# Kernel optimization log

Measured on AMD Instinct MI355X. Metric: run time of the kernel, lower is better.

The kernel has to match this reference:

```python
import jax, jax.numpy as jnp
import numpy as np

N = 100000      # nodes
E = 1600000     # edges
G = 2000        # molecules (graphs)
F = 40          # node features
FE = 16         # edge features
H = 64          # conv width
HM = 128        # mlp width
C = 2           # classes
NEG_SLOPE = 0.01
BN_EPS = 1e-5


def leaky(x):
    return jnp.where(x >= 0, x, NEG_SLOPE * x)


def batch_norm(x, g, b):
    # training-mode BatchNorm over the node axis (biased variance, eps=1e-5)
    m = jnp.mean(x, axis=0)
    v = jnp.var(x, axis=0)
    return (x - m) * jax.lax.rsqrt(v + BN_EPS) * g + b


def setup_inputs() -> dict:
    key = jax.random.key(0)
    ks = iter(jax.random.split(key, 100))

    def nrm(shape, s=1.0):
        return jax.random.normal(next(ks), shape, dtype=jnp.float32) * s

    inp = {}
    inp["x"] = nrm((N, F))
    inp["edge_index"] = jax.random.randint(next(ks), (2, E), 0, N, dtype=jnp.int32)
    inp["edge_attr"] = nrm((E, FE))
    inp["batch"] = jnp.repeat(jnp.arange(G, dtype=jnp.int32), N // G)

    dims = [(F, H), (H, H), (H, H)]
    for i, (ci, co) in enumerate(dims):
        inp[f"conv{i}_eps"] = jnp.zeros((1,), dtype=jnp.float32)
        inp[f"conv{i}_We"] = nrm((FE, ci), 1.0 / np.sqrt(FE))
        inp[f"conv{i}_be"] = nrm((ci,), 0.05)
        inp[f"conv{i}_W1"] = nrm((ci, co), 1.0 / np.sqrt(ci))
        inp[f"conv{i}_b1"] = nrm((co,), 0.05)
        inp[f"conv{i}_g1"] = 1.0 + nrm((co,), 0.05)
        inp[f"conv{i}_bt1"] = nrm((co,), 0.05)
        inp[f"conv{i}_W2"] = nrm((co, co), 1.0 / np.sqrt(co))
        inp[f"conv{i}_b2"] = nrm((co,), 0.05)
        inp[f"bn{i}_g"] = 1.0 + nrm((co,), 0.05)
        inp[f"bn{i}_b"] = nrm((co,), 0.05)

    inp["mlp0_W"] = nrm((2 * H, HM), 1.0 / np.sqrt(2 * H))
    inp["mlp0_b"] = nrm((HM,), 0.05)
    inp["mlp1_W"] = nrm((HM, HM), 1.0 / np.sqrt(HM))
    inp["mlp1_b"] = nrm((HM,), 0.05)
    inp["final_W"] = nrm((HM, C), 1.0 / np.sqrt(HM))
    inp["final_b"] = nrm((C,), 0.05)
    return inp


def _forward(x, edge_attr, edge_index, batch, convs, mlps, final_W, final_b):
    src, dst = edge_index[0], edge_index[1]
    for (eps, We, be, W1, b1, g1, bt1, W2, b2, bg, bb) in convs:
        # GINEConv: msg = relu(x_src + lin_edge(edge_attr)); scatter-add to dst
        e = edge_attr @ We + be                    # [E, in]
        msg = jax.nn.relu(x[src] + e)              # gather + fuse
        agg = jax.ops.segment_sum(msg, dst, num_segments=x.shape[0])
        h = (1.0 + eps) * x + agg
        # conv nn: Linear -> BatchNorm -> LeakyReLU -> Linear
        h = batch_norm(h @ W1 + b1, g1, bt1)
        h = leaky(h) @ W2 + b2
        # outer BatchNorm + LeakyReLU
        x = leaky(batch_norm(h, bg, bb))
    # global_add_pool then repeat_interleave by per-mol counts == pool[batch]
    pool = jax.ops.segment_sum(x, batch, num_segments=G)
    x = jnp.concatenate([x, pool[batch]], axis=1)  # [N, 2H]
    for (W, b) in mlps:
        x = leaky(x @ W + b)  # dropout is identity in eval mode
    return x @ final_W + final_b


def reference(x, edge_index, edge_attr, batch,
              conv0_eps, conv0_We, conv0_be, conv0_W1, conv0_b1, conv0_g1, conv0_bt1, conv0_W2, conv0_b2, bn0_g, bn0_b,
              conv1_eps, conv1_We, conv1_be, conv1_W1, conv1_b1, conv1_g1, conv1_bt1, conv1_W2, conv1_b2, bn1_g, bn1_b,
              conv2_eps, conv2_We, conv2_be, conv2_W1, conv2_b1, conv2_g1, conv2_bt1, conv2_W2, conv2_b2, bn2_g, bn2_b,
              mlp0_W, mlp0_b, mlp1_W, mlp1_b, final_W, final_b):
    convs = [
        (conv0_eps, conv0_We, conv0_be, conv0_W1, conv0_b1, conv0_g1, conv0_bt1, conv0_W2, conv0_b2, bn0_g, bn0_b),
        (conv1_eps, conv1_We, conv1_be, conv1_W1, conv1_b1, conv1_g1, conv1_bt1, conv1_W2, conv1_b2, bn1_g, bn1_b),
        (conv2_eps, conv2_We, conv2_be, conv2_W1, conv2_b1, conv2_g1, conv2_bt1, conv2_W2, conv2_b2, bn2_g, bn2_b),
    ]
    mlps = [(mlp0_W, mlp0_b), (mlp1_W, mlp1_b)]
    return _forward(x, edge_attr, edge_index, batch, convs, mlps, final_W, final_b)
```

## Files before the change

### kernel.cpp

```cpp
#include <hip/hip_runtime.h>


#define N_  100000
#define E_  1600000
#define G_  2000
#define SCAN_NB 196
#define NBLK 1563

typedef _Float16 half2v __attribute__((ext_vector_type(2)));

__device__ __forceinline__ float leaky_(float z) { return z >= 0.f ? z : 0.01f * z; }

__device__ __forceinline__ half2v u2h(unsigned u) {
    union { unsigned u; half2v h; } c; c.u = u; return c.h;
}

__device__ __forceinline__ float dot2_(half2v a, half2v b, float c) {
#if __has_builtin(__builtin_amdgcn_fdot2)
    return __builtin_amdgcn_fdot2(a, b, c, false);
#else
    return c + (float)a.x * (float)b.x + (float)a.y * (float)b.y;
#endif
}

__global__ __launch_bounds__(256) void hist_rank_kernel(
    const int* __restrict__ dst, int* __restrict__ cnt, int* __restrict__ rank)
{
#pragma unroll 4
    for (int e = blockIdx.x * 256 + threadIdx.x; e < E_; e += gridDim.x * 256)
        rank[e] = atomicAdd(&cnt[dst[e]], 1);
}

__global__ __launch_bounds__(256) void scanA(
    const int* __restrict__ cnt, int* __restrict__ blocksum)
{
    __shared__ int s[256];
    const int t = threadIdx.x, b = blockIdx.x;
    const int i0 = (b * 256 + t) * 2;
    int v = 0;
    if (i0 < N_) v += cnt[i0];
    if (i0 + 1 < N_) v += cnt[i0 + 1];
    s[t] = v; __syncthreads();
    for (int o = 128; o > 0; o >>= 1) { if (t < o) s[t] += s[t + o]; __syncthreads(); }
    if (t == 0) blocksum[b] = s[0];
}

__global__ __launch_bounds__(256) void scanB(
    const int* __restrict__ blocksum, int* __restrict__ blockpref)
{
    __shared__ int s[256];
    const int t = threadIdx.x;
    int v = (t < SCAN_NB) ? blocksum[t] : 0;
    s[t] = v; __syncthreads();
    for (int o = 1; o < 256; o <<= 1) {
        int u = (t >= o) ? s[t - o] : 0;
        __syncthreads(); s[t] += u; __syncthreads();
    }
    blockpref[t] = s[t] - v;
}

__global__ __launch_bounds__(256) void scanC(
    const int* __restrict__ cnt, int* __restrict__ off,
    const int* __restrict__ blockpref)
{
    __shared__ int s[256];
    const int t = threadIdx.x, b = blockIdx.x;
    const int i0 = (b * 256 + t) * 2;
    int v0 = (i0 < N_) ? cnt[i0] : 0;
    int v1 = (i0 + 1 < N_) ? cnt[i0 + 1] : 0;
    int pv = v0 + v1;
    s[t] = pv; __syncthreads();
    for (int o = 1; o < 256; o <<= 1) {
        int u = (t >= o) ? s[t - o] : 0;
        __syncthreads(); s[t] += u; __syncthreads();
    }
    int run = blockpref[b] + s[t] - pv;
    if (i0 < N_) {
        off[i0] = run; run += v0;
        if (i0 + 1 < N_) off[i0 + 1] = run;
    }
    if (b == 0 && t == 0) off[N_] = E_;
}

__global__ __launch_bounds__(256) void place_kernel(
    const int* __restrict__ src, const int* __restrict__ dst,
    const int* __restrict__ rank, const int* __restrict__ off,
    const float* __restrict__ edge_attr,
    int* __restrict__ src_s, unsigned short* __restrict__ ea_h)
{
#pragma unroll 2
    for (int e = blockIdx.x * 256 + threadIdx.x; e < E_; e += gridDim.x * 256) {
        const int p = off[dst[e]] + rank[e];
        src_s[p] = src[e];
        const float4* __restrict__ ea = (const float4*)(edge_attr + (size_t)e * 16);
        float4 a0 = ea[0], a1 = ea[1], a2 = ea[2], a3 = ea[3];
        union { uint4 u4[2]; half2v h[8]; } cv;
        cv.h[0] = half2v{(_Float16)a0.x, (_Float16)a0.y};
        cv.h[1] = half2v{(_Float16)a0.z, (_Float16)a0.w};
        cv.h[2] = half2v{(_Float16)a1.x, (_Float16)a1.y};
        cv.h[3] = half2v{(_Float16)a1.z, (_Float16)a1.w};
        cv.h[4] = half2v{(_Float16)a2.x, (_Float16)a2.y};
        cv.h[5] = half2v{(_Float16)a2.z, (_Float16)a2.w};
        cv.h[6] = half2v{(_Float16)a3.x, (_Float16)a3.y};
        cv.h[7] = half2v{(_Float16)a3.z, (_Float16)a3.w};
        uint4* __restrict__ eo = (uint4*)(ea_h + (size_t)p * 16);
        eo[0] = cv.u4[0]; eo[1] = cv.u4[1];
    }
}

#define DPW 13
#define CHUNK 32

template<int CI>
__global__ __launch_bounds__(256, 4) void agg_sorted(
    const unsigned short* __restrict__ ea_h,
    const int* __restrict__ src_s,
    const int* __restrict__ off,
    const float* __restrict__ We, const float* __restrict__ be,
    const float* __restrict__ x, float* __restrict__ agg)
{
    __shared__ __align__(16) unsigned s_ea[4][2][CHUNK * 8];
    __shared__ int s_src[4][2][CHUNK];
    const int t = threadIdx.x;
    const int lane = t & 63;
    const int w = t >> 6;
    const int wid = __builtin_amdgcn_readfirstlane(blockIdx.x * 4 + w);

    half2v wh[8];
#pragma unroll
    for (int k = 0; k < 8; ++k) wh[k] = half2v{(_Float16)0.f, (_Float16)0.f};
    float beL = 0.f;
    if (lane < CI) {
#pragma unroll
        for (int k = 0; k < 8; ++k)
            wh[k] = half2v{(_Float16)We[(2 * k) * CI + lane],
                           (_Float16)We[(2 * k + 1) * CI + lane]};
        beL = be[lane];
    }
    const int ln = (lane < CI) ? lane : 0;

    const int d0 = wid * DPW;
    if (d0 >= N_) return;
    const int d1 = min(d0 + DPW, N_);
    const int pw0 = off[d0];
    const int pw1 = off[d1];

    int d = d0;
    int e1 = off[d0 + 1];
    float acc = 0.f;
    int buf = 0;

    {
        const int m = min(CHUNK, pw1 - pw0);
        uint4 v = make_uint4(0, 0, 0, 0);
        if (lane < m * 2) v = ((const uint4*)(ea_h + (size_t)pw0 * 16))[lane];
        *(uint4*)&s_ea[w][0][lane * 4] = v;
        if (lane < CHUNK)
            s_src[w][0][lane] = (lane < m) ? src_s[pw0 + lane] : 0;
    }
    __builtin_amdgcn_wave_barrier();

    for (int cp = pw0; cp < pw1; cp += CHUNK) {
        const int m = min(CHUNK, pw1 - cp);
        const int np = cp + CHUNK;
        const int nm = min(CHUNK, pw1 - np);

        uint4 pre = make_uint4(0, 0, 0, 0);
        int psrc = 0;
        if (nm > 0) {
            if (lane < nm * 2) pre = ((const uint4*)(ea_h + (size_t)np * 16))[lane];
            if (lane < nm) psrc = src_s[np + lane];
        }

        float xr[CHUNK];
#pragma unroll
        for (int i = 0; i < CHUNK; ++i) {
            const int s = s_src[w][buf][i];
            xr[i] = x[(size_t)s * CI + ln];
        }

#pragma unroll
        for (int i = 0; i < CHUNK; ++i) {
            if (i >= m) break;
            while (cp + i == e1) {
                if (lane < CI) agg[(size_t)d * CI + lane] = acc;
                acc = 0.f; ++d;
                e1 = off[d + 1];
            }
            const unsigned* er = &s_ea[w][buf][i * 8];
            uint4 e0 = *(const uint4*)&er[0];
            uint4 e2 = *(const uint4*)&er[4];
            float dotv = beL;
            dotv = dot2_(u2h(e0.x), wh[0], dotv);
            dotv = dot2_(u2h(e0.y), wh[1], dotv);
            dotv = dot2_(u2h(e0.z), wh[2], dotv);
            dotv = dot2_(u2h(e0.w), wh[3], dotv);
            dotv = dot2_(u2h(e2.x), wh[4], dotv);
            dotv = dot2_(u2h(e2.y), wh[5], dotv);
            dotv = dot2_(u2h(e2.z), wh[6], dotv);
            dotv = dot2_(u2h(e2.w), wh[7], dotv);
            float mm = xr[i] + dotv;
            acc += (mm > 0.f ? mm : 0.f);
        }

        if (nm > 0) {
            *(uint4*)&s_ea[w][buf ^ 1][lane * 4] = pre;
            if (lane < CHUNK) s_src[w][buf ^ 1][lane] = psrc;
        }
        __builtin_amdgcn_wave_barrier();
        buf ^= 1;
    }

    while (d < d1) {
        if (lane < CI) agg[(size_t)d * CI + lane] = acc;
        acc = 0.f; ++d;
    }
}

template<int CI, int MODE>
__global__ __launch_bounds__(256, 4) void node_gemm(
    const float* __restrict__ in,
    const float* __restrict__ agg,
    const float* __restrict__ eps,
    const float* __restrict__ g1,
    const float* __restrict__ bt1,
    const float* __restrict__ stIn,
    const float* __restrict__ W, const float* __restrict__ bias_,
    float* __restrict__ outbuf, float* __restrict__ partial)
{
    __shared__ __align__(16) float a_lds[64][CI + 4];
    __shared__ __align__(16) float w_lds[CI][68];
    __shared__ float s_sc[64], s_sh[64];
    const int t = threadIdx.x;
    const int n0 = blockIdx.x * 64;
    constexpr int QR = CI / 4;

    if (MODE == 1) {
        if (t < 64) {
            float mean = stIn[t] * (1.0f / N_);
            float var  = stIn[64 + t] * (1.0f / N_) - mean * mean;
            float sc = g1[t] * rsqrtf(var + 1e-5f);
            s_sc[t] = sc;
            s_sh[t] = bt1[t] - mean * sc;
        }
        __syncthreads();
    }

    if (MODE == 0) {
        const float hs = 1.0f + eps[0];
        for (int f = t; f < 64 * QR; f += 256) {
            int i = f / QR, q = f - i * QR;
            int n = n0 + i;
            float4 val = make_float4(0.f, 0.f, 0.f, 0.f);
            if (n < N_) {
                float4 xa = *(const float4*)&in[(size_t)n * CI + q * 4];
                float4 ag = *(const float4*)&agg[(size_t)n * CI + q * 4];
                val = make_float4(hs * xa.x + ag.x, hs * xa.y + ag.y,
                                  hs * xa.z + ag.z, hs * xa.w + ag.w);
            }
            *(float4*)&a_lds[i][q * 4] = val;
        }
    } else {
        for (int f = t; f < 64 * QR; f += 256) {
            int i = f / QR, q = f - i * QR;
            int n = n0 + i;
            float4 val = make_float4(0.f, 0.f, 0.f, 0.f);
            if (n < N_) {
                float4 uv = *(const float4*)&in[(size_t)n * CI + q * 4];
                int c = q * 4;
                val = make_float4(leaky_(uv.x * s_sc[c]     + s_sh[c]),
                                  leaky_(uv.y * s_sc[c + 1] + s_sh[c + 1]),
                                  leaky_(uv.z * s_sc[c + 2] + s_sh[c + 2]),
                                  leaky_(uv.w * s_sc[c + 3] + s_sh[c + 3]));
            }
            *(float4*)&a_lds[i][q * 4] = val;
        }
    }
    for (int f = t; f < CI * 16; f += 256) {
        int k = f >> 4, cq = f & 15;
        *(float4*)&w_lds[k][cq * 4] = *(const float4*)&W[k * 64 + cq * 4];
    }
    __syncthreads();

    const int tr = t & 15;
    const int c0 = (t >> 4) * 4;
    float acc[4][4] = {};
#pragma unroll 2
    for (int k = 0; k < CI; k += 4) {
        float ar[4][4];
#pragma unroll
        for (int j = 0; j < 4; ++j)
            *(float4*)&ar[j][0] = *(const float4*)&a_lds[tr + 16 * j][k];
#pragma unroll
        for (int kk = 0; kk < 4; ++kk) {
            float4 b = *(const float4*)&w_lds[k + kk][c0];
#pragma unroll
            for (int j = 0; j < 4; ++j) {
                acc[j][0] += ar[j][kk] * b.x;
                acc[j][1] += ar[j][kk] * b.y;
                acc[j][2] += ar[j][kk] * b.z;
                acc[j][3] += ar[j][kk] * b.w;
            }
        }
    }

    const float4 bb = *(const float4*)&bias_[c0];
    const float bias[4] = { bb.x, bb.y, bb.z, bb.w };
    float ls[4] = {}, lq[4] = {};
#pragma unroll
    for (int j = 0; j < 4; ++j) {
        int n = n0 + tr + 16 * j;
        if (n < N_) {
            float o[4];
#pragma unroll
            for (int cc = 0; cc < 4; ++cc) {
                o[cc] = acc[j][cc] + bias[cc];
                ls[cc] += o[cc];
                lq[cc] += o[cc] * o[cc];
            }
            *(float4*)&outbuf[(size_t)n * 64 + c0] = make_float4(o[0], o[1], o[2], o[3]);
        }
    }
#pragma unroll
    for (int m = 1; m <= 8; m <<= 1) {
#pragma unroll
        for (int cc = 0; cc < 4; ++cc) {
            ls[cc] += __shfl_xor(ls[cc], m);
            lq[cc] += __shfl_xor(lq[cc], m);
        }
    }
    if (tr == 0) {
#pragma unroll
        for (int cc = 0; cc < 4; ++cc) {
            partial[(size_t)(c0 + cc) * NBLK + blockIdx.x]      = ls[cc];
            partial[(size_t)(64 + c0 + cc) * NBLK + blockIdx.x] = lq[cc];
        }
    }
}

__global__ __launch_bounds__(256) void finalize_stats(
    const float* __restrict__ partial, float* __restrict__ stats)
{
    const int c = blockIdx.x;
    const int t = threadIdx.x;
    float s = 0.f;
    for (int b = t; b < NBLK; b += 256) s += partial[(size_t)c * NBLK + b];
    __shared__ float red[256];
    red[t] = s; __syncthreads();
    for (int o = 128; o > 0; o >>= 1) { if (t < o) red[t] += red[t + o]; __syncthreads(); }
    if (t == 0) stats[c] = red[0];
}

__global__ __launch_bounds__(256) void apply_bn_leaky(
    const float* __restrict__ v, const float* __restrict__ st,
    const float* __restrict__ g, const float* __restrict__ b,
    float* __restrict__ xout)
{
    size_t idx = ((size_t)blockIdx.x * 256 + threadIdx.x) * 4;
    if (idx >= (size_t)N_ * 64) return;
    int c0 = (int)(idx & 63);
    float4 vv = *(const float4*)&v[idx];
    float vi[4] = { vv.x, vv.y, vv.z, vv.w };
    float o[4];
#pragma unroll
    for (int cc = 0; cc < 4; ++cc) {
        int c = c0 + cc;
        float mean = st[c] * (1.0f / N_);
        float var  = st[64 + c] * (1.0f / N_) - mean * mean;
        float sc = g[c] * rsqrtf(var + 1e-5f);
        float sh = b[c] - mean * sc;
        o[cc] = leaky_(vi[cc] * sc + sh);
    }
    *(float4*)&xout[idx] = make_float4(o[0], o[1], o[2], o[3]);
}

__global__ __launch_bounds__(256) void pool_kernel(
    const float* __restrict__ x, float* __restrict__ pool)
{
    const int c = threadIdx.x & 63;
    const int g = blockIdx.x * 4 + (threadIdx.x >> 6);
    const float* p = x + (size_t)g * 50 * 64 + c;
    float s = 0.f;
#pragma unroll
    for (int j = 0; j < 50; ++j) s += p[(size_t)j * 64];
    pool[(size_t)g * 64 + c] = s;
}

__global__ __launch_bounds__(256) void pool_mlp0(
    const float* __restrict__ pool, const float* __restrict__ W0,
    const float* __restrict__ b0, float* __restrict__ g0)
{
    const int t = threadIdx.x;
    const int g = blockIdx.x * 2 + (t >> 7);
    const int c = t & 127;
    float s = b0[c];
    const float* pr = pool + (size_t)g * 64;
#pragma unroll 4
    for (int k = 0; k < 64; ++k)
        s += pr[k] * W0[(size_t)(64 + k) * 128 + c];
    g0[(size_t)g * 128 + c] = s;
}

__global__ __launch_bounds__(256, 2) void mlp_kernel(
    const float* __restrict__ x, const float* __restrict__ g0,
    const float* __restrict__ W0,
    const float* __restrict__ W1, const float* __restrict__ b1,
    const float* __restrict__ Wf, const float* __restrict__ bf,
    float* __restrict__ out)
{
    __shared__ __align__(16) float a_lds[128][132];
    __shared__ __align__(16) float w_lds[16][132];
    __shared__ __align__(16) float sWfT[2][128];
    __shared__ int sbid[128];
    const int t = threadIdx.x;
    const int n0 = blockIdx.x * 128;

    for (int f = t; f < 128 * 16; f += 256) {
        int i = f >> 4, q = f & 15;
        int n = n0 + i;
        float4 val = make_float4(0.f, 0.f, 0.f, 0.f);
        if (n < N_) val = *(const float4*)&x[(size_t)n * 64 + q * 4];
        *(float4*)&a_lds[i][q * 4] = val;
    }
    if (t < 128) {
        int n = n0 + t;
        sbid[t] = (n < N_) ? (n / 50) : (G_ - 1);
        sWfT[0][t] = Wf[t * 2];
        sWfT[1][t] = Wf[t * 2 + 1];
    }

    const int tr = t & 15;
    const int c0 = (t >> 4) * 8;
    float acc[8][8];

#pragma unroll
    for (int j = 0; j < 8; ++j)
#pragma unroll
        for (int cc = 0; cc < 8; ++cc) acc[j][cc] = 0.f;

    for (int kc = 0; kc < 64; kc += 16) {
        __syncthreads();
        for (int f = t; f < 16 * 32; f += 256) {
            int k = f >> 5, cq = f & 31;
            *(float4*)&w_lds[k][cq * 4] = *(const float4*)&W0[(size_t)(kc + k) * 128 + cq * 4];
        }
        __syncthreads();
        for (int k = 0; k < 16; k += 4) {
            float ar[8][4];
#pragma unroll
            for (int j = 0; j < 8; ++j)
                *(float4*)&ar[j][0] = *(const float4*)&a_lds[tr + 16 * j][kc + k];
#pragma unroll
            for (int kk = 0; kk < 4; ++kk) {
                float4 bA = *(const float4*)&w_lds[k + kk][c0];
                float4 bB = *(const float4*)&w_lds[k + kk][c0 + 4];
#pragma unroll
                for (int j = 0; j < 8; ++j) {
                    acc[j][0] += ar[j][kk] * bA.x;
                    acc[j][1] += ar[j][kk] * bA.y;
                    acc[j][2] += ar[j][kk] * bA.z;
                    acc[j][3] += ar[j][kk] * bA.w;
                    acc[j][4] += ar[j][kk] * bB.x;
                    acc[j][5] += ar[j][kk] * bB.y;
                    acc[j][6] += ar[j][kk] * bB.z;
                    acc[j][7] += ar[j][kk] * bB.w;
                }
            }
        }
    }
    __syncthreads();
#pragma unroll
    for (int j = 0; j < 8; ++j) {
        int row = tr + 16 * j;
        const float* gr = g0 + (size_t)sbid[row] * 128;
        float4 gA = *(const float4*)&gr[c0];
        float4 gB = *(const float4*)&gr[c0 + 4];
        float o[8] = { acc[j][0] + gA.x, acc[j][1] + gA.y, acc[j][2] + gA.z, acc[j][3] + gA.w,
                       acc[j][4] + gB.x, acc[j][5] + gB.y, acc[j][6] + gB.z, acc[j][7] + gB.w };
#pragma unroll
        for (int cc = 0; cc < 8; ++cc) o[cc] = leaky_(o[cc]);
        *(float4*)&a_lds[row][c0]     = make_float4(o[0], o[1], o[2], o[3]);
        *(float4*)&a_lds[row][c0 + 4] = make_float4(o[4], o[5], o[6], o[7]);
    }

#pragma unroll
    for (int j = 0; j < 8; ++j)
#pragma unroll
        for (int cc = 0; cc < 8; ++cc) acc[j][cc] = 0.f;

    for (int kc = 0; kc < 128; kc += 16) {
        __syncthreads();
        for (int f = t; f < 16 * 32; f += 256) {
            int k = f >> 5, cq = f & 31;
            *(float4*)&w_lds[k][cq * 4] = *(const float4*)&W1[(size_t)(kc + k) * 128 + cq * 4];
        }
        __syncthreads();
        for (int k = 0; k < 16; k += 4) {
            float ar[8][4];
#pragma unroll
            for (int j = 0; j < 8; ++j)
                *(float4*)&ar[j][0] = *(const float4*)&a_lds[tr + 16 * j][kc + k];
#pragma unroll
            for (int kk = 0; kk < 4; ++kk) {
                float4 bA = *(const float4*)&w_lds[k + kk][c0];
                float4 bB = *(const float4*)&w_lds[k + kk][c0 + 4];
#pragma unroll
                for (int j = 0; j < 8; ++j) {
                    acc[j][0] += ar[j][kk] * bA.x;
                    acc[j][1] += ar[j][kk] * bA.y;
                    acc[j][2] += ar[j][kk] * bA.z;
                    acc[j][3] += ar[j][kk] * bA.w;
                    acc[j][4] += ar[j][kk] * bB.x;
                    acc[j][5] += ar[j][kk] * bB.y;
                    acc[j][6] += ar[j][kk] * bB.z;
                    acc[j][7] += ar[j][kk] * bB.w;
                }
            }
        }
    }
    __syncthreads();
    {
        float4 bb0 = *(const float4*)&b1[c0];
        float4 bb1 = *(const float4*)&b1[c0 + 4];
        float bias[8] = { bb0.x, bb0.y, bb0.z, bb0.w, bb1.x, bb1.y, bb1.z, bb1.w };
#pragma unroll
        for (int j = 0; j < 8; ++j) {
            int row = tr + 16 * j;
            float o[8];
#pragma unroll
            for (int cc = 0; cc < 8; ++cc) o[cc] = leaky_(acc[j][cc] + bias[cc]);
            *(float4*)&a_lds[row][c0]     = make_float4(o[0], o[1], o[2], o[3]);
            *(float4*)&a_lds[row][c0 + 4] = make_float4(o[4], o[5], o[6], o[7]);
        }
    }
    __syncthreads();

    {
        int i = t >> 1, c = t & 1;
        int n = n0 + i;
        if (n < N_) {
            float s = bf[c];
            for (int k = 0; k < 128; k += 4) {
                float4 av = *(const float4*)&a_lds[i][k];
                float4 wv = *(const float4*)&sWfT[c][k];
                s += av.x * wv.x + av.y * wv.y + av.z * wv.z + av.w * wv.w;
            }
            out[(size_t)n * 2 + c] = s;
        }
    }
}

extern "C" void kernel_launch(void* const* d_in, const int* in_sizes, int n_in,
                              void* d_out, int out_size, void* d_ws, size_t ws_size,
                              hipStream_t stream)
{
    (void)in_sizes; (void)n_in; (void)out_size; (void)ws_size;

    const float* x0    = (const float*)d_in[0];
    const int*   eidx  = (const int*)d_in[1];
    const float* eattr = (const float*)d_in[2];
    const float* L[3][11];
    for (int l = 0; l < 3; ++l)
        for (int j = 0; j < 11; ++j)
            L[l][j] = (const float*)d_in[4 + l * 11 + j];
    const float* mlp0W = (const float*)d_in[37];
    const float* mlp0b = (const float*)d_in[38];
    const float* mlp1W = (const float*)d_in[39];
    const float* mlp1b = (const float*)d_in[40];
    const float* finW  = (const float*)d_in[41];
    const float* finb  = (const float*)d_in[42];
    float* out = (float*)d_out;

    float* ws    = (float*)d_ws;
    float* agg   = ws;
    float* u     = agg  + (size_t)N_ * 64;
    float* xbuf  = u    + (size_t)N_ * 64;
    float* pool  = xbuf + (size_t)N_ * 64;
    float* g0    = pool + (size_t)G_ * 64;
    float* stats = g0   + (size_t)G_ * 128;
    float* partial = stats + 768;
    int*   off   = (int*)(partial + 128 * NBLK);
    int*   cnt   = off + (N_ + 2);
    int*   bsum  = cnt + N_;
    int*   bpref = bsum + 256;
    int*   rank  = bpref + 256;
    int*   src_s = rank + E_;
    unsigned short* ea_h = (unsigned short*)((((uintptr_t)(src_s + E_)) + 63) & ~(uintptr_t)63);
    float* v = agg;

    const int* src = eidx;
    const int* dst = eidx + E_;
    const int GB = NBLK;

    hipMemsetAsync(cnt, 0, (size_t)N_ * sizeof(int), stream);
    hist_rank_kernel<<<2048, 256, 0, stream>>>(dst, cnt, rank);
    scanA<<<SCAN_NB, 256, 0, stream>>>(cnt, bsum);
    scanB<<<1, 256, 0, stream>>>(bsum, bpref);
    scanC<<<SCAN_NB, 256, 0, stream>>>(cnt, off, bpref);
    place_kernel<<<2048, 256, 0, stream>>>(src, dst, rank, off, eattr, src_s, ea_h);

    const int AGGB = ((N_ + DPW - 1) / DPW + 3) / 4 + 1;

    for (int l = 0; l < 3; ++l) {
        float* s1 = stats + (2 * l) * 128;
        float* s2 = stats + (2 * l + 1) * 128;
        if (l == 0) {
            agg_sorted<40><<<AGGB, 256, 0, stream>>>(ea_h, src_s, off, L[0][1], L[0][2], x0, agg);
            node_gemm<40, 0><<<GB, 256, 0, stream>>>(x0, agg, L[0][0], nullptr, nullptr, nullptr,
                                                     L[0][3], L[0][4], u, partial);
        } else {
            agg_sorted<64><<<AGGB, 256, 0, stream>>>(ea_h, src_s, off, L[l][1], L[l][2], xbuf, agg);
            node_gemm<64, 0><<<GB, 256, 0, stream>>>(xbuf, agg, L[l][0], nullptr, nullptr, nullptr,
                                                     L[l][3], L[l][4], u, partial);
        }
        finalize_stats<<<128, 256, 0, stream>>>(partial, s1);
        node_gemm<64, 1><<<GB, 256, 0, stream>>>(u, nullptr, nullptr, L[l][5], L[l][6], s1,
                                                 L[l][7], L[l][8], v, partial);
        finalize_stats<<<128, 256, 0, stream>>>(partial, s2);
        apply_bn_leaky<<<6250, 256, 0, stream>>>(v, s2, L[l][9], L[l][10], xbuf);
    }

    pool_kernel<<<G_ / 4, 256, 0, stream>>>(xbuf, pool);
    pool_mlp0<<<G_ / 2, 256, 0, stream>>>(pool, mlp0W, mlp0b, g0);
    mlp_kernel<<<(N_ + 127) / 128, 256, 0, stream>>>(xbuf, g0, mlp0W,
                                                     mlp1W, mlp1b, finW, finb, out);
}
```

Measured before the change: 905.3 us.

## Fuse BN+leaky into consumers and gather edge attributes via sorted edge ids

The standalone apply_bn_leaky pass is removed; its batch-norm and leaky ReLU are now applied on the fly wherever the pre-BN activations are read (aggregation, the node GEMM, pool and the MLP). The placement kernel no longer builds a dst-sorted fp16 copy of the edge attributes. It writes (src, edge id) pairs, and the aggregation kernel gathers the fp32 edge attributes by id, converts them to fp16 and prefetches one chunk ahead. This saves a full N×64 read/write per layer plus the sorted attribute copy. In exchange, BN math is redone for every gathered neighbour, and each layer makes random, twice-as-large fp32 reads of the edge attributes.

```diff
diff --git a/kernel.cpp b/kernel.cpp
--- a/kernel.cpp
+++ b/kernel.cpp
@@ -85,39 +85,28 @@
 __global__ __launch_bounds__(256) void place_kernel(
     const int* __restrict__ src, const int* __restrict__ dst,
     const int* __restrict__ rank, const int* __restrict__ off,
-    const float* __restrict__ edge_attr,
-    int* __restrict__ src_s, unsigned short* __restrict__ ea_h)
-{
-#pragma unroll 2
+    int2* __restrict__ se)
+{
+#pragma unroll 4
     for (int e = blockIdx.x * 256 + threadIdx.x; e < E_; e += gridDim.x * 256) {
         const int p = off[dst[e]] + rank[e];
-        src_s[p] = src[e];
-        const float4* __restrict__ ea = (const float4*)(edge_attr + (size_t)e * 16);
-        float4 a0 = ea[0], a1 = ea[1], a2 = ea[2], a3 = ea[3];
-        union { uint4 u4[2]; half2v h[8]; } cv;
-        cv.h[0] = half2v{(_Float16)a0.x, (_Float16)a0.y};
-        cv.h[1] = half2v{(_Float16)a0.z, (_Float16)a0.w};
-        cv.h[2] = half2v{(_Float16)a1.x, (_Float16)a1.y};
-        cv.h[3] = half2v{(_Float16)a1.z, (_Float16)a1.w};
-        cv.h[4] = half2v{(_Float16)a2.x, (_Float16)a2.y};
-        cv.h[5] = half2v{(_Float16)a2.z, (_Float16)a2.w};
-        cv.h[6] = half2v{(_Float16)a3.x, (_Float16)a3.y};
-        cv.h[7] = half2v{(_Float16)a3.z, (_Float16)a3.w};
-        uint4* __restrict__ eo = (uint4*)(ea_h + (size_t)p * 16);
-        eo[0] = cv.u4[0]; eo[1] = cv.u4[1];
+        se[p] = make_int2(src[e], e);
     }
 }
 
 #define DPW 13
 #define CHUNK 32
 
-template<int CI>
+template<int CI, int APPLY_BN>
 __global__ __launch_bounds__(256, 4) void agg_sorted(
-    const unsigned short* __restrict__ ea_h,
-    const int* __restrict__ src_s,
+    const float* __restrict__ edge_attr,
+    const int2* __restrict__ se,
     const int* __restrict__ off,
     const float* __restrict__ We, const float* __restrict__ be,
-    const float* __restrict__ x, float* __restrict__ agg)
+    const float* __restrict__ x,
+    const float* __restrict__ stIn,
+    const float* __restrict__ bng, const float* __restrict__ bnb,
+    float* __restrict__ agg)
 {
     __shared__ __align__(16) unsigned s_ea[4][2][CHUNK * 8];
     __shared__ int s_src[4][2][CHUNK];
@@ -129,13 +118,19 @@
     half2v wh[8];
 #pragma unroll
     for (int k = 0; k < 8; ++k) wh[k] = half2v{(_Float16)0.f, (_Float16)0.f};
-    float beL = 0.f;
+    float beL = 0.f, scL = 1.f, shL = 0.f;
     if (lane < CI) {
 #pragma unroll
         for (int k = 0; k < 8; ++k)
             wh[k] = half2v{(_Float16)We[(2 * k) * CI + lane],
                            (_Float16)We[(2 * k + 1) * CI + lane]};
         beL = be[lane];
+        if (APPLY_BN) {
+            float mean = stIn[lane] * (1.0f / N_);
+            float var  = stIn[64 + lane] * (1.0f / N_) - mean * mean;
+            scL = bng[lane] * rsqrtf(var + 1e-5f);
+            shL = bnb[lane] - mean * scL;
+        }
     }
     const int ln = (lane < CI) ? lane : 0;
 
@@ -144,19 +139,40 @@
     const int d1 = min(d0 + DPW, N_);
     const int pw0 = off[d0];
     const int pw1 = off[d1];
+    if (pw0 >= pw1) {
+        for (int d = d0; d < d1; ++d)
+            if (lane < CI) agg[(size_t)d * CI + lane] = 0.f;
+        return;
+    }
 
     int d = d0;
     int e1 = off[d0 + 1];
     float acc = 0.f;
     int buf = 0;
+    const int r = lane >> 1;
+    const int hf = lane & 1;
 
     {
-        const int m = min(CHUNK, pw1 - pw0);
-        uint4 v = make_uint4(0, 0, 0, 0);
-        if (lane < m * 2) v = ((const uint4*)(ea_h + (size_t)pw0 * 16))[lane];
-        *(uint4*)&s_ea[w][0][lane * 4] = v;
-        if (lane < CHUNK)
-            s_src[w][0][lane] = (lane < m) ? src_s[pw0 + lane] : 0;
+        const int m0 = min(CHUNK, pw1 - pw0);
+        int2 t0 = make_int2(0, 0);
+        if (lane < m0) t0 = se[pw0 + lane];
+        int e = __shfl(t0.y, r);
+        if (r >= m0) e = 0;
+        const float4* ep = (const float4*)(edge_attr + (size_t)e * 16 + hf * 8);
+        float4 f0 = ep[0], f1 = ep[1];
+        union { uint4 u; half2v h[4]; } cv;
+        cv.h[0] = half2v{(_Float16)f0.x, (_Float16)f0.y};
+        cv.h[1] = half2v{(_Float16)f0.z, (_Float16)f0.w};
+        cv.h[2] = half2v{(_Float16)f1.x, (_Float16)f1.y};
+        cv.h[3] = half2v{(_Float16)f1.z, (_Float16)f1.w};
+        *(uint4*)&s_ea[w][0][r * 8 + hf * 4] = cv.u;
+        if (lane < CHUNK) s_src[w][0][lane] = (lane < m0) ? t0.x : 0;
+    }
+    int2 pse = make_int2(0, 0);
+    {
+        const int np = pw0 + CHUNK;
+        const int nm = min(CHUNK, pw1 - np);
+        if (nm > 0 && lane < nm) pse = se[np + lane];
     }
     __builtin_amdgcn_wave_barrier();
 
@@ -164,21 +180,26 @@
         const int m = min(CHUNK, pw1 - cp);
         const int np = cp + CHUNK;
         const int nm = min(CHUNK, pw1 - np);
-
-        uint4 pre = make_uint4(0, 0, 0, 0);
-        int psrc = 0;
+        const int np2 = cp + 2 * CHUNK;
+        const int nm2 = min(CHUNK, pw1 - np2);
+
+        float4 g0 = make_float4(0.f, 0.f, 0.f, 0.f), g1 = g0;
         if (nm > 0) {
-            if (lane < nm * 2) pre = ((const uint4*)(ea_h + (size_t)np * 16))[lane];
-            if (lane < nm) psrc = src_s[np + lane];
-        }
+            int ge = __shfl(pse.y, r);
+            if (r >= nm) ge = 0;
+            const float4* ep = (const float4*)(edge_attr + (size_t)ge * 16 + hf * 8);
+            g0 = ep[0]; g1 = ep[1];
+        }
+        int2 nse = make_int2(0, 0);
+        if (nm2 > 0 && lane < nm2) nse = se[np2 + lane];
 
         float xr[CHUNK];
 #pragma unroll
         for (int i = 0; i < CHUNK; ++i) {
             const int s = s_src[w][buf][i];
-            xr[i] = x[(size_t)s * CI + ln];
-        }
-
+            float raw = x[(size_t)s * CI + ln];
+            xr[i] = APPLY_BN ? leaky_(raw * scL + shL) : raw;
+        }
 #pragma unroll
         for (int i = 0; i < CHUNK; ++i) {
             if (i >= m) break;
@@ -204,9 +225,15 @@
         }
 
         if (nm > 0) {
-            *(uint4*)&s_ea[w][buf ^ 1][lane * 4] = pre;
-            if (lane < CHUNK) s_src[w][buf ^ 1][lane] = psrc;
-        }
+            union { uint4 u; half2v h[4]; } cv;
+            cv.h[0] = half2v{(_Float16)g0.x, (_Float16)g0.y};
+            cv.h[1] = half2v{(_Float16)g0.z, (_Float16)g0.w};
+            cv.h[2] = half2v{(_Float16)g1.x, (_Float16)g1.y};
+            cv.h[3] = half2v{(_Float16)g1.z, (_Float16)g1.w};
+            *(uint4*)&s_ea[w][buf ^ 1][r * 8 + hf * 4] = cv.u;
+            if (lane < CHUNK) s_src[w][buf ^ 1][lane] = (lane < nm) ? pse.x : 0;
+        }
+        pse = nse;
         __builtin_amdgcn_wave_barrier();
         buf ^= 1;
     }
@@ -217,7 +244,7 @@
     }
 }
 
-template<int CI, int MODE>
+template<int CI, int MODE, int BNIN>
 __global__ __launch_bounds__(256, 4) void node_gemm(
     const float* __restrict__ in,
     const float* __restrict__ agg,
@@ -235,7 +262,7 @@
     const int n0 = blockIdx.x * 64;
     constexpr int QR = CI / 4;
 
-    if (MODE == 1) {
+    if (MODE == 1 || BNIN) {
         if (t < 64) {
             float mean = stIn[t] * (1.0f / N_);
             float var  = stIn[64 + t] * (1.0f / N_) - mean * mean;
@@ -255,6 +282,13 @@
             if (n < N_) {
                 float4 xa = *(const float4*)&in[(size_t)n * CI + q * 4];
                 float4 ag = *(const float4*)&agg[(size_t)n * CI + q * 4];
+                if (BNIN) {
+                    int c = q * 4;
+                    xa.x = leaky_(xa.x * s_sc[c]     + s_sh[c]);
+                    xa.y = leaky_(xa.y * s_sc[c + 1] + s_sh[c + 1]);
+                    xa.z = leaky_(xa.z * s_sc[c + 2] + s_sh[c + 2]);
+                    xa.w = leaky_(xa.w * s_sc[c + 3] + s_sh[c + 3]);
+                }
                 val = make_float4(hs * xa.x + ag.x, hs * xa.y + ag.y,
                                   hs * xa.z + ag.z, hs * xa.w + ag.w);
             }
@@ -351,38 +385,21 @@
     if (t == 0) stats[c] = red[0];
 }
 
-__global__ __launch_bounds__(256) void apply_bn_leaky(
+__global__ __launch_bounds__(256) void pool_kernel(
     const float* __restrict__ v, const float* __restrict__ st,
-    const float* __restrict__ g, const float* __restrict__ b,
-    float* __restrict__ xout)
-{
-    size_t idx = ((size_t)blockIdx.x * 256 + threadIdx.x) * 4;
-    if (idx >= (size_t)N_ * 64) return;
-    int c0 = (int)(idx & 63);
-    float4 vv = *(const float4*)&v[idx];
-    float vi[4] = { vv.x, vv.y, vv.z, vv.w };
-    float o[4];
-#pragma unroll
-    for (int cc = 0; cc < 4; ++cc) {
-        int c = c0 + cc;
-        float mean = st[c] * (1.0f / N_);
-        float var  = st[64 + c] * (1.0f / N_) - mean * mean;
-        float sc = g[c] * rsqrtf(var + 1e-5f);
-        float sh = b[c] - mean * sc;
-        o[cc] = leaky_(vi[cc] * sc + sh);
-    }
-    *(float4*)&xout[idx] = make_float4(o[0], o[1], o[2], o[3]);
-}
-
-__global__ __launch_bounds__(256) void pool_kernel(
-    const float* __restrict__ x, float* __restrict__ pool)
+    const float* __restrict__ bg, const float* __restrict__ bb,
+    float* __restrict__ pool)
 {
     const int c = threadIdx.x & 63;
     const int g = blockIdx.x * 4 + (threadIdx.x >> 6);
-    const float* p = x + (size_t)g * 50 * 64 + c;
+    float mean = st[c] * (1.0f / N_);
+    float var  = st[64 + c] * (1.0f / N_) - mean * mean;
+    float sc = bg[c] * rsqrtf(var + 1e-5f);
+    float sh = bb[c] - mean * sc;
+    const float* p = v + (size_t)g * 50 * 64 + c;
     float s = 0.f;
 #pragma unroll
-    for (int j = 0; j < 50; ++j) s += p[(size_t)j * 64];
+    for (int j = 0; j < 50; ++j) s += leaky_(p[(size_t)j * 64] * sc + sh);
     pool[(size_t)g * 64 + c] = s;
 }
 
@@ -402,7 +419,9 @@
 }
 
 __global__ __launch_bounds__(256, 2) void mlp_kernel(
-    const float* __restrict__ x, const float* __restrict__ g0,
+    const float* __restrict__ v, const float* __restrict__ st,
+    const float* __restrict__ bg, const float* __restrict__ bb,
+    const float* __restrict__ g0,
     const float* __restrict__ W0,
     const float* __restrict__ W1, const float* __restrict__ b1,
     const float* __restrict__ Wf, const float* __restrict__ bf,
@@ -411,15 +430,32 @@
     __shared__ __align__(16) float a_lds[128][132];
     __shared__ __align__(16) float w_lds[16][132];
     __shared__ __align__(16) float sWfT[2][128];
+    __shared__ float s_scm[64], s_shm[64];
     __shared__ int sbid[128];
     const int t = threadIdx.x;
     const int n0 = blockIdx.x * 128;
+
+    if (t < 64) {
+        float mean = st[t] * (1.0f / N_);
+        float var  = st[64 + t] * (1.0f / N_) - mean * mean;
+        float sc = bg[t] * rsqrtf(var + 1e-5f);
+        s_scm[t] = sc;
+        s_shm[t] = bb[t] - mean * sc;
+    }
+    __syncthreads();
 
     for (int f = t; f < 128 * 16; f += 256) {
         int i = f >> 4, q = f & 15;
         int n = n0 + i;
         float4 val = make_float4(0.f, 0.f, 0.f, 0.f);
-        if (n < N_) val = *(const float4*)&x[(size_t)n * 64 + q * 4];
+        if (n < N_) {
+            float4 xv = *(const float4*)&v[(size_t)n * 64 + q * 4];
+            int c = q * 4;
+            val = make_float4(leaky_(xv.x * s_scm[c]     + s_shm[c]),
+                              leaky_(xv.y * s_scm[c + 1] + s_shm[c + 1]),
+                              leaky_(xv.z * s_scm[c + 2] + s_shm[c + 2]),
+                              leaky_(xv.w * s_scm[c + 3] + s_shm[c + 3]));
+        }
         *(float4*)&a_lds[i][q * 4] = val;
     }
     if (t < 128) {
@@ -572,10 +608,10 @@
     float* out = (float*)d_out;
 
     float* ws    = (float*)d_ws;
-    float* agg   = ws;
-    float* u     = agg  + (size_t)N_ * 64;
-    float* xbuf  = u    + (size_t)N_ * 64;
-    float* pool  = xbuf + (size_t)N_ * 64;
+    float* P0    = ws;
+    float* P1    = P0 + (size_t)N_ * 64;
+    float* P2    = P1 + (size_t)N_ * 64;
+    float* pool  = P2 + (size_t)N_ * 64;
     float* g0    = pool + (size_t)G_ * 64;
     float* stats = g0   + (size_t)G_ * 128;
     float* partial = stats + 768;
@@ -584,9 +620,7 @@
     int*   bsum  = cnt + N_;
     int*   bpref = bsum + 256;
     int*   rank  = bpref + 256;
-    int*   src_s = rank + E_;
-    unsigned short* ea_h = (unsigned short*)((((uintptr_t)(src_s + E_)) + 63) & ~(uintptr_t)63);
-    float* v = agg;
+    int2*  se    = (int2*)(rank + E_);
 
     const int* src = eidx;
     const int* dst = eidx + E_;
@@ -597,7 +631,7 @@
     scanA<<<SCAN_NB, 256, 0, stream>>>(cnt, bsum);
     scanB<<<1, 256, 0, stream>>>(bsum, bpref);
     scanC<<<SCAN_NB, 256, 0, stream>>>(cnt, off, bpref);
-    place_kernel<<<2048, 256, 0, stream>>>(src, dst, rank, off, eattr, src_s, ea_h);
+    place_kernel<<<2048, 256, 0, stream>>>(src, dst, rank, off, se);
 
     const int AGGB = ((N_ + DPW - 1) / DPW + 3) / 4 + 1;
 
@@ -605,23 +639,26 @@
         float* s1 = stats + (2 * l) * 128;
         float* s2 = stats + (2 * l + 1) * 128;
         if (l == 0) {
-            agg_sorted<40><<<AGGB, 256, 0, stream>>>(ea_h, src_s, off, L[0][1], L[0][2], x0, agg);
-            node_gemm<40, 0><<<GB, 256, 0, stream>>>(x0, agg, L[0][0], nullptr, nullptr, nullptr,
-                                                     L[0][3], L[0][4], u, partial);
+            agg_sorted<40, 0><<<AGGB, 256, 0, stream>>>(eattr, se, off, L[0][1], L[0][2],
+                                                        x0, nullptr, nullptr, nullptr, P0);
+            node_gemm<40, 0, 0><<<GB, 256, 0, stream>>>(x0, P0, L[0][0], nullptr, nullptr, nullptr,
+                                                        L[0][3], L[0][4], P1, partial);
         } else {
-            agg_sorted<64><<<AGGB, 256, 0, stream>>>(ea_h, src_s, off, L[l][1], L[l][2], xbuf, agg);
-            node_gemm<64, 0><<<GB, 256, 0, stream>>>(xbuf, agg, L[l][0], nullptr, nullptr, nullptr,
-                                                     L[l][3], L[l][4], u, partial);
+            float* sp = stats + (2 * l - 1) * 128;
+            agg_sorted<64, 1><<<AGGB, 256, 0, stream>>>(eattr, se, off, L[l][1], L[l][2],
+                                                        P2, sp, L[l - 1][9], L[l - 1][10], P0);
+            node_gemm<64, 0, 1><<<GB, 256, 0, stream>>>(P2, P0, L[l][0], L[l - 1][9], L[l - 1][10], sp,
+                                                        L[l][3], L[l][4], P1, partial);
         }
         finalize_stats<<<128, 256, 0, stream>>>(partial, s1);
-        node_gemm<64, 1><<<GB, 256, 0, stream>>>(u, nullptr, nullptr, L[l][5], L[l][6], s1,
-                                                 L[l][7], L[l][8], v, partial);
+        node_gemm<64, 1, 0><<<GB, 256, 0, stream>>>(P1, nullptr, nullptr, L[l][5], L[l][6], s1,
+                                                    L[l][7], L[l][8], P2, partial);
         finalize_stats<<<128, 256, 0, stream>>>(partial, s2);
-        apply_bn_leaky<<<6250, 256, 0, stream>>>(v, s2, L[l][9], L[l][10], xbuf);
-    }
-
-    pool_kernel<<<G_ / 4, 256, 0, stream>>>(xbuf, pool);
+    }
+
+    float* sF = stats + 5 * 128;
+    pool_kernel<<<G_ / 4, 256, 0, stream>>>(P2, sF, L[2][9], L[2][10], pool);
     pool_mlp0<<<G_ / 2, 256, 0, stream>>>(pool, mlp0W, mlp0b, g0);
-    mlp_kernel<<<(N_ + 127) / 128, 256, 0, stream>>>(xbuf, g0, mlp0W,
+    mlp_kernel<<<(N_ + 127) / 128, 256, 0, stream>>>(P2, sF, L[2][9], L[2][10], g0, mlp0W,
                                                      mlp1W, mlp1b, finW, finb, out);
 }
```

Measured after the change: 892.2 us. No clear change (-1.4%).
